# Performance work log

Hardware: AMD Instinct MI355X
Metric: run time of the kernel (lower is better)

## Reference

```python
import jax, jax.numpy as jnp
import numpy as np

B, T, C, H = 8, 1024, 768, 12
HD = C // H  # 64, even for RoPE
ROPE_THETA = 10000.0


def precompute_freqs_cis(dim, end, theta=ROPE_THETA):
    # [end, dim//2, 2] with (cos, sin) in last axis
    freqs = 1.0 / theta ** (jnp.arange(0, dim // 2).astype(jnp.float32) / (dim // 2))
    t = jnp.arange(end)
    f = jnp.outer(t, freqs)
    return jnp.stack([jnp.cos(f), jnp.sin(f)], axis=-1)


def apply_rope(x, fc):
    # x: [B,T,H,hd]; fc: [T,1,hd//2,2] (broadcasts over B and H)
    xr = x.reshape(*x.shape[:-1], -1, 2)
    x_re, x_im = xr[..., 0], xr[..., 1]
    cos, sin = fc[..., 0], fc[..., 1]
    out_re = x_re * cos - x_im * sin
    out_im = x_re * sin + x_im * cos
    return jnp.stack([out_re, out_im], axis=-1).reshape(x.shape)


def setup_inputs() -> dict:
    key = jax.random.key(0)
    k0, k1, k2 = jax.random.split(key, 3)
    x = jax.random.normal(k0, (B, T, C), jnp.float32)
    Wqkv = jax.random.normal(k1, (C, 3 * C), jnp.float32) * 0.02
    bqkv = jnp.zeros((3 * C,), jnp.float32)
    Wproj = jax.random.normal(k2, (C, C), jnp.float32) * 0.02
    bproj = jnp.zeros((C,), jnp.float32)
    mask = jnp.tril(jnp.ones((T, T), jnp.int32))  # causal
    return {"x": x, "Wqkv": Wqkv, "bqkv": bqkv, "Wproj": Wproj, "bproj": bproj, "mask": mask}


def reference(x, Wqkv, bqkv, Wproj, bproj, mask):
    B_, T_, C_ = x.shape
    qkv = (x @ Wqkv + bqkv).reshape(B_, T_, 3, H, HD)
    q, k, v = qkv[:, :, 0], qkv[:, :, 1], qkv[:, :, 2]  # each [B,T,H,hd]
    fc = precompute_freqs_cis(HD, T_)[:, None]  # [T,1,hd//2,2]
    q = apply_rope(q, fc)
    k = apply_rope(k, fc)
    scale = 1.0 / jnp.sqrt(jnp.float32(HD))
    attn = jnp.einsum('bthd,bkhd->bhtk', q, k) * scale  # [B,H,T,T]
    neg = jnp.finfo(attn.dtype).min
    attn = jnp.where(mask[None, None, :, :] == 0, neg, attn)
    attn = jax.nn.softmax(attn, axis=-1)
    out = jnp.einsum('bhtk,bkhd->bthd', attn, v).reshape(B_, T_, C_)
    return out @ Wproj + bproj
```

## Files before the change

kernel.cpp:

```cpp
#include <hip/hip_runtime.h>
#include <cstdint>
#include <cstddef>
#include <cstring>

#define BB 8
#define TT 1024
#define CC 768
#define NH 12
#define HD 64

using bf16x8 = __attribute__((ext_vector_type(8))) short;
using f32x4  = __attribute__((ext_vector_type(4))) float;

static __device__ __forceinline__ short f2bf(float f) {
    uint32_t u;
    __builtin_memcpy(&u, &f, 4);
    u += 0x7FFFu + ((u >> 16) & 1u);
    return (short)(u >> 16);
}

static __device__ __forceinline__ uint32_t bfpack(float lo, float hi) {
    return (uint32_t)(uint16_t)f2bf(lo) | ((uint32_t)(uint16_t)f2bf(hi) << 16);
}

__global__ __launch_bounds__(256)
void prep_kernel(const float* __restrict__ x, const float* __restrict__ Wqkv,
                 const float* __restrict__ Wproj,
                 short* __restrict__ WqkvT, short* __restrict__ WprojT,
                 short* __restrict__ xb, float2* __restrict__ fc) {
    __shared__ float tile[32][33];
    const int tid = threadIdx.x;
    int bid = blockIdx.x;
    if (bid < 2304) {
        const float* in;
        short* out;
        int Cdim, bx, by;
        if (bid < 1728) { in = Wqkv; out = WqkvT; Cdim = 2304; bx = bid % 72; by = bid / 72; }
        else { int b2 = bid - 1728; in = Wproj; out = WprojT; Cdim = 768; bx = b2 % 24; by = b2 / 24; }
        int tx = tid & 31, ty = tid >> 5;
        int c0 = bx * 32, r0 = by * 32;
#pragma unroll
        for (int i = 0; i < 4; i++)
            tile[ty + 8 * i][tx] = in[(size_t)(r0 + ty + 8 * i) * Cdim + c0 + tx];
        __syncthreads();
#pragma unroll
        for (int i = 0; i < 4; i++)
            out[(size_t)(c0 + ty + 8 * i) * 768 + r0 + tx] = f2bf(tile[tx][ty + 8 * i]);
    } else if (bid < 5376) {
        int i = ((bid - 2304) * 256 + tid) * 8;
        float4 f0 = *(const float4*)(x + i);
        float4 f1 = *(const float4*)(x + i + 4);
        bf16x8 h;
        h[0] = f2bf(f0.x); h[1] = f2bf(f0.y); h[2] = f2bf(f0.z); h[3] = f2bf(f0.w);
        h[4] = f2bf(f1.x); h[5] = f2bf(f1.y); h[6] = f2bf(f1.z); h[7] = f2bf(f1.w);
        *(bf16x8*)(xb + i) = h;
    } else {
        int idx = (bid - 5376) * 256 + tid;
        int t = idx >> 5, p = idx & 31;
        float freq = powf(10000.0f, -(float)p / 32.0f);
        float a = (float)t * freq;
        fc[idx] = make_float2(cosf(a), sinf(a));
    }
}

template <int EPI>
__global__ __launch_bounds__(256, 2)
void gemm_kernel(const short* __restrict__ Agl, const short* __restrict__ BT,
                 const float* __restrict__ bias,
                 short* __restrict__ Qb, short* __restrict__ Kb, short* __restrict__ VT,
                 const float2* __restrict__ fc, float* __restrict__ out) {
    __shared__ __align__(16) short smem_s[4 * 128 * 64];
    short (*As)[128 * 64] = (short(*)[128 * 64])smem_s;
    short (*Bs)[128 * 64] = (short(*)[128 * 64])(smem_s + 2 * 128 * 64);
    const int tid = threadIdx.x;
    const int lane = tid & 63, wid = tid >> 6;
    const int g = lane >> 4, c = lane & 15;
    const int wm = wid >> 1, wn = wid & 1;

    const int nx = gridDim.x;
    const int bid = blockIdx.y * nx + blockIdx.x;
    const int cpx = (nx * gridDim.y) >> 3;
    const int swz = (bid & 7) * cpx + (bid >> 3);
    const int m0 = (swz / nx) * 128, n0 = (swz % nx) * 128;

    const int srow = lane >> 2;
    const int sch = lane & 3;
    const short* Ab0 = Agl + (size_t)(m0 + wid * 32 + srow) * 768 + sch * 8;
    const short* Bb0 = BT  + (size_t)(n0 + wid * 32 + srow) * 768 + sch * 8;

    const f32x4 zero4 = {0.f, 0.f, 0.f, 0.f};
    f32x4 acc[4][4];
#pragma unroll
    for (int i = 0; i < 4; i++)
#pragma unroll
        for (int j = 0; j < 4; j++) acc[i][j] = zero4;

    bf16x8 rA[4], rB[4];
#define LOAD(kt)                                                               \
    {                                                                          \
        size_t ko = (size_t)(kt) * 64;                                         \
        _Pragma("unroll")                                                      \
        for (int q = 0; q < 2; q++)                                            \
            _Pragma("unroll")                                                  \
            for (int h = 0; h < 2; h++) {                                      \
                rA[q * 2 + h] = *(const bf16x8*)(Ab0 + (size_t)q * 16 * 768 + ko + h * 32); \
                rB[q * 2 + h] = *(const bf16x8*)(Bb0 + (size_t)q * 16 * 768 + ko + h * 32); \
            }                                                                  \
    }
#define WRITE(buf)                                                             \
    {                                                                          \
        _Pragma("unroll")                                                      \
        for (int q = 0; q < 2; q++)                                            \
            _Pragma("unroll")                                                  \
            for (int h = 0; h < 2; h++) {                                      \
                int row = wid * 32 + q * 16 + srow;                            \
                int ci = sch + h * 4;                                          \
                int idx = row * 64 + ((ci ^ (row & 7)) * 8);                   \
                *(bf16x8*)&As[buf][idx] = rA[q * 2 + h];                       \
                *(bf16x8*)&Bs[buf][idx] = rB[q * 2 + h];                       \
            }                                                                  \
    }
#define COMPUTE(buf)                                                           \
    {                                                                          \
        _Pragma("unroll")                                                      \
        for (int kk = 0; kk < 2; kk++) {                                       \
            bf16x8 af[4], bfr[4];                                              \
            _Pragma("unroll")                                                  \
            for (int mi = 0; mi < 4; mi++) {                                   \
                int row = wm * 64 + mi * 16 + c;                               \
                af[mi] = *(const bf16x8*)&As[buf][row * 64 + (((kk * 4 + g) ^ (row & 7)) * 8)]; \
            }                                                                  \
            _Pragma("unroll")                                                  \
            for (int ni = 0; ni < 4; ni++) {                                   \
                int row = wn * 64 + ni * 16 + c;                               \
                bfr[ni] = *(const bf16x8*)&Bs[buf][row * 64 + (((kk * 4 + g) ^ (row & 7)) * 8)]; \
            }                                                                  \
            __builtin_amdgcn_s_setprio(1);                                     \
            _Pragma("unroll")                                                  \
            for (int mi = 0; mi < 4; mi++)                                     \
                _Pragma("unroll")                                              \
                for (int ni = 0; ni < 4; ni++)                                 \
                    acc[mi][ni] = __builtin_amdgcn_mfma_f32_16x16x32_bf16(     \
                        af[mi], bfr[ni], acc[mi][ni], 0, 0, 0);                \
            __builtin_amdgcn_s_setprio(0);                                     \
        }                                                                      \
    }

    LOAD(0);
    WRITE(0);
    __syncthreads();

#pragma unroll 1
    for (int t2 = 0; t2 < 12; t2 += 2) {
        LOAD(t2 + 1);
        COMPUTE(0);
        __syncthreads();
        WRITE(1);
        __syncthreads();
        if (t2 + 2 < 12) {
            LOAD(t2 + 2);
            COMPUTE(1);
            __syncthreads();
            WRITE(0);
            __syncthreads();
        } else {
            COMPUTE(1);
        }
    }
    __syncthreads();

    if (EPI == 0) {
        uint32_t* LD = (uint32_t*)smem_s;
#pragma unroll
        for (int ni = 0; ni < 4; ni++) {
            int nl = wn * 64 + ni * 16 + c;
            int n = n0 + nl;
            float bv = bias[n];
            int part = (n >= 1536) ? 2 : (n >= 768 ? 1 : 0);
            int d = (n - part * 768) & 63;
#pragma unroll
            for (int mi = 0; mi < 4; mi++) {
#pragma unroll
                for (int r = 0; r < 4; r++) {
                    int ml = wm * 64 + mi * 16 + g * 4 + r;
                    float v = acc[mi][ni][r] + bv;
                    float pv = __shfl_xor(v, 1);
                    if (!(c & 1)) {
                        float o0, o1;
                        if (part < 2) {
                            int t = (m0 + ml) & 1023;
                            float2 cs = fc[t * 32 + (d >> 1)];
                            o0 = v * cs.x - pv * cs.y;
                            o1 = v * cs.y + pv * cs.x;
                            if (part == 0) { o0 *= 0.125f; o1 *= 0.125f; }
                        } else { o0 = v; o1 = pv; }
                        LD[ml * 64 + ((nl >> 1) ^ (((ml >> 2) & 3) << 3))] = bfpack(o0, o1);
                    }
                }
            }
        }
        __syncthreads();
        if (n0 >= 1536) {
            int n0r = n0 - 1536;
            int h0 = n0r >> 6;
            int wc = tid & 63;
            int seg = tid >> 2 >> 4;
            int h = h0 + (wc >> 5);
            int d0 = (2 * wc) & 63;
            int b = m0 >> 10, t0r = m0 & 1023;
            uint32_t wlo[16], whi[16];
#pragma unroll
            for (int j2 = 0; j2 < 16; j2++) {
                int mlA = seg * 32 + 2 * j2;
                int mlB = mlA + 1;
                uint32_t wa = LD[mlA * 64 + (wc ^ (((mlA >> 2) & 3) << 3))];
                uint32_t wb = LD[mlB * 64 + (wc ^ (((mlB >> 2) & 3) << 3))];
                wlo[j2] = (wa & 0xFFFFu) | (wb << 16);
                whi[j2] = (wa >> 16) | (wb & 0xFFFF0000u);
            }
            short* p0 = VT + ((size_t)(b * NH + h) * HD + d0) * TT + t0r + seg * 32;
            short* p1 = p0 + TT;
#pragma unroll
            for (int k = 0; k < 4; k++) {
                int4 v0, v1;
                __builtin_memcpy(&v0, &wlo[k * 4], 16);
                __builtin_memcpy(&v1, &whi[k * 4], 16);
                *(int4*)(p0 + k * 8) = v0;
                *(int4*)(p1 + k * 8) = v1;
            }
        } else {
#pragma unroll
            for (int p = 0; p < 8; p++) {
                int ml = p * 16 + (tid >> 4);
                int wc = (tid & 15) * 4;
                int4 dat = *(const int4*)&LD[ml * 64 + (wc ^ (((ml >> 2) & 3) << 3))];
                int n = n0 + wc * 2;
                int part = (n >= 768) ? 1 : 0;
                int rem = n - part * 768;
                int h = rem >> 6, d = rem & 63;
                int m = m0 + ml, b = m >> 10, t = m & 1023;
                short* dst = (part == 0 ? Qb : Kb)
                             + (((size_t)b * NH + h) * TT + t) * HD + d;
                *(int4*)dst = dat;
            }
        }
    } else {
        float* LDf = (float*)smem_s;
#pragma unroll
        for (int mi = 0; mi < 4; mi++)
#pragma unroll
            for (int ni = 0; ni < 4; ni++) {
                int nl = wn * 64 + ni * 16 + c;
                float bv = bias[n0 + nl];
#pragma unroll
                for (int r = 0; r < 4; r++) {
                    int ml = wm * 64 + mi * 16 + g * 4 + r;
                    LDf[ml * 128 + (nl ^ (r << 3))] = acc[mi][ni][r] + bv;
                }
            }
        __syncthreads();
#pragma unroll
        for (int p = 0; p < 8; p++) {
            int ml = p * 16 + (tid >> 4);
            int rr = (ml & 3) << 3;
            int wc4 = (tid & 15) * 8;
            const float* rp = &LDf[ml * 128 + (wc4 ^ rr)];
            float4 f0 = *(const float4*)rp;
            float4 f1 = *(const float4*)(rp + 4);
            float* dst = out + (size_t)(m0 + ml) * CC + n0 + wc4;
            *(float4*)dst = f0;
            *(float4*)(dst + 4) = f1;
        }
    }
#undef LOAD
#undef WRITE
#undef COMPUTE
}

__global__ __launch_bounds__(256)
void attn_kernel(const short* __restrict__ Qb, const short* __restrict__ Kb,
                 const short* __restrict__ VT, short* __restrict__ Ob) {
    __shared__ uint32_t Pt[4][32][32];
    __shared__ uint32_t ot[128 * 32];
    const int tid = threadIdx.x, lane = tid & 63, wid = tid >> 6;
    const int g = lane >> 4, c = lane & 15;
    const int bh = blockIdx.x, qb = 7 - (int)blockIdx.y;
    const int b = bh / NH, h = bh % NH;
    const short* Qp = Qb + (size_t)bh * TT * HD;
    const short* Kp = Kb + (size_t)bh * TT * HD;
    const short* Vp = VT + (size_t)bh * TT * HD;
    const int q0 = qb * 128 + wid * 32;
    const int sw = (c & 7) << 2;

    bf16x8 qf[2][2];
#pragma unroll
    for (int qs = 0; qs < 2; qs++)
#pragma unroll
        for (int kh = 0; kh < 2; kh++)
            qf[qs][kh] = *(const bf16x8*)(Qp + (size_t)(q0 + qs * 16 + c) * HD + kh * 32 + g * 8);

    const f32x4 zero4 = {0.f, 0.f, 0.f, 0.f};
    f32x4 o[2][4];
#pragma unroll
    for (int qs = 0; qs < 2; qs++)
#pragma unroll
        for (int dt = 0; dt < 4; dt++) o[qs][dt] = zero4;
    float mrun[2] = {-1e30f, -1e30f}, lrun[2] = {0.f, 0.f};

    const int t0max = ((q0 + 31) >> 6) << 6;
    for (int t0 = 0; t0 <= t0max; t0 += 64) {
        f32x4 st[2][4];
#pragma unroll
        for (int nt = 0; nt < 4; nt++) {
            const short* kp = Kp + (size_t)(t0 + nt * 16 + c) * HD + g * 8;
            bf16x8 k0 = *(const bf16x8*)kp;
            bf16x8 k1 = *(const bf16x8*)(kp + 32);
#pragma unroll
            for (int qs = 0; qs < 2; qs++) {
                f32x4 z = zero4;
                __builtin_amdgcn_s_setprio(1);
                z = __builtin_amdgcn_mfma_f32_16x16x32_bf16(k0, qf[qs][0], z, 0, 0, 0);
                z = __builtin_amdgcn_mfma_f32_16x16x32_bf16(k1, qf[qs][1], z, 0, 0, 0);
                __builtin_amdgcn_s_setprio(0);
                st[qs][nt] = z;
            }
        }
        bf16x8 vf[2][4];
#pragma unroll
        for (int blk = 0; blk < 2; blk++)
#pragma unroll
            for (int dt = 0; dt < 4; dt++)
                vf[blk][dt] = *(const bf16x8*)(Vp + (size_t)(dt * 16 + c) * TT + t0 + blk * 32 + g * 8);
        if (t0 + 63 > q0) {
#pragma unroll
            for (int qs = 0; qs < 2; qs++) {
                int q = q0 + qs * 16 + c;
#pragma unroll
                for (int nt = 0; nt < 4; nt++)
#pragma unroll
                    for (int r = 0; r < 4; r++)
                        if (t0 + nt * 16 + g * 4 + r > q) st[qs][nt][r] = -1e30f;
            }
        }
#pragma unroll
        for (int qs = 0; qs < 2; qs++) {
            float mx = st[qs][0][0];
#pragma unroll
            for (int nt = 0; nt < 4; nt++)
#pragma unroll
                for (int r = 0; r < 4; r++) mx = fmaxf(mx, st[qs][nt][r]);
            mx = fmaxf(mx, __shfl_xor(mx, 16));
            mx = fmaxf(mx, __shfl_xor(mx, 32));
            float mnew = fmaxf(mrun[qs], mx);
            float al = __expf(mrun[qs] - mnew);
            mrun[qs] = mnew;
            float sm = 0.f;
#pragma unroll
            for (int nt = 0; nt < 4; nt++)
#pragma unroll
                for (int r = 0; r < 4; r++) {
                    float e = __expf(st[qs][nt][r] - mnew);
                    st[qs][nt][r] = e;
                    sm += e;
                }
            sm += __shfl_xor(sm, 16);
            sm += __shfl_xor(sm, 32);
            lrun[qs] = lrun[qs] * al + sm;
#pragma unroll
            for (int dt = 0; dt < 4; dt++) {
                o[qs][dt][0] *= al; o[qs][dt][1] *= al;
                o[qs][dt][2] *= al; o[qs][dt][3] *= al;
            }
            int row = qs * 16 + c;
#pragma unroll
            for (int nt = 0; nt < 4; nt++) {
                uint32_t w0 = bfpack(st[qs][nt][0], st[qs][nt][1]);
                uint32_t w1 = bfpack(st[qs][nt][2], st[qs][nt][3]);
                int wa = nt * 8 + 2 * g;
                Pt[wid][row][wa ^ sw]       = w0;
                Pt[wid][row][(wa + 1) ^ sw] = w1;
            }
        }
#pragma unroll
        for (int qs = 0; qs < 2; qs++) {
            int row = qs * 16 + c;
#pragma unroll
            for (int blk = 0; blk < 2; blk++) {
                bf16x8 pf = *(const bf16x8*)&Pt[wid][row][(blk * 16 + 4 * g) ^ sw];
                __builtin_amdgcn_s_setprio(1);
#pragma unroll
                for (int dt = 0; dt < 4; dt++)
                    o[qs][dt] = __builtin_amdgcn_mfma_f32_16x16x32_bf16(
                        vf[blk][dt], pf, o[qs][dt], 0, 0, 0);
                __builtin_amdgcn_s_setprio(0);
            }
        }
    }

#pragma unroll
    for (int qs = 0; qs < 2; qs++) {
        float inv = 1.0f / lrun[qs];
        int ql = wid * 32 + qs * 16 + c;
#pragma unroll
        for (int dt = 0; dt < 4; dt++) {
            uint32_t w0 = bfpack(o[qs][dt][0] * inv, o[qs][dt][1] * inv);
            uint32_t w1 = bfpack(o[qs][dt][2] * inv, o[qs][dt][3] * inv);
            int jc0 = dt * 8 + 2 * g;
            int jc1 = jc0 + 1;
            ot[ql * 32 + ((((jc0 >> 2) ^ (c & 7)) << 2) | (jc0 & 3))] = w0;
            ot[ql * 32 + ((((jc1 >> 2) ^ (c & 7)) << 2) | (jc1 & 3))] = w1;
        }
    }
    __syncthreads();
#pragma unroll
    for (int p = 0; p < 4; p++) {
        int q = (tid >> 3) + 32 * p;
        int jb = tid & 7;
        const uint32_t* src = &ot[q * 32 + ((jb ^ (q & 7)) << 2)];
        int4 w = *(const int4*)src;
        *(int4*)(Ob + ((size_t)b * TT + qb * 128 + q) * CC + h * HD + jb * 8) = w;
    }
}

extern "C" void kernel_launch(void* const* d_in, const int* in_sizes, int n_in,
                              void* d_out, int out_size, void* d_ws, size_t ws_size,
                              hipStream_t stream) {
    const float* x     = (const float*)d_in[0];
    const float* Wqkv  = (const float*)d_in[1];
    const float* bqkv  = (const float*)d_in[2];
    const float* Wproj = (const float*)d_in[3];
    const float* bproj = (const float*)d_in[4];

    char* ws = (char*)d_ws;
    short*  WqkvT  = (short*)(ws);
    short*  WprojT = (short*)(ws + 3538944);
    float2* fc     = (float2*)(ws + 3538944 + 1179648);
    short*  Qb     = (short*)(ws + 4980736);
    short*  Kb     = (short*)(ws + 4980736 + 1 * 12582912);
    short*  VOb    = (short*)(ws + 4980736 + 2 * 12582912);
    short*  VbT    = (short*)(ws + 4980736 + 3 * 12582912);
    short*  xb     = VOb;
    float*  out    = (float*)d_out;

    hipLaunchKernelGGL(prep_kernel, dim3(5504), dim3(256), 0, stream,
                       x, Wqkv, Wproj, WqkvT, WprojT, xb, fc);
    hipLaunchKernelGGL((gemm_kernel<0>), dim3(18, 64), dim3(256), 0, stream,
                       xb, WqkvT, bqkv, Qb, Kb, VbT, fc, (float*)nullptr);
    hipLaunchKernelGGL(attn_kernel, dim3(96, 8), dim3(256), 0, stream, Qb, Kb, VbT, VOb);
    hipLaunchKernelGGL((gemm_kernel<1>), dim3(6, 64), dim3(256), 0, stream,
                       VOb, WprojT, bproj,
                       (short*)nullptr, (short*)nullptr, (short*)nullptr,
                       (const float2*)nullptr, out);
}
```

Measured before the change: 164.3 us.

## Load GEMM B-operand fragments directly from global into registers, skip LDS

The GEMM kernel no longer stages the weight (B) tile through shared memory. Each wave loads its own MFMA B fragments straight from global memory into registers, and only A is double-buffered in LDS. That halves the LDS footprint for the QKV GEMM, which now targets 4 blocks per CU instead of 2. In exchange, B data is no longer shared between the two waves that use the same columns, so global/L2 traffic rises, register pressure grows, and the global loads are issued in the same iteration they are consumed, exposing their latency.

Result: slower. 366.1 us (+122.8%).

```diff
diff --git a/kernel.cpp b/kernel.cpp
--- a/kernel.cpp
+++ b/kernel.cpp
@@ -64,14 +64,13 @@
 }
 
 template <int EPI>
-__global__ __launch_bounds__(256, 2)
+__global__ __launch_bounds__(256, EPI == 0 ? 4 : 2)
 void gemm_kernel(const short* __restrict__ Agl, const short* __restrict__ BT,
                  const float* __restrict__ bias,
                  short* __restrict__ Qb, short* __restrict__ Kb, short* __restrict__ VT,
                  const float2* __restrict__ fc, float* __restrict__ out) {
-    __shared__ __align__(16) short smem_s[4 * 128 * 64];
-    short (*As)[128 * 64] = (short(*)[128 * 64])smem_s;
-    short (*Bs)[128 * 64] = (short(*)[128 * 64])(smem_s + 2 * 128 * 64);
+    __shared__ __align__(16) char smem_c[EPI == 0 ? 32768 : 65536];
+    short (*As)[128 * 64] = (short(*)[128 * 64])smem_c;
     const int tid = threadIdx.x;
     const int lane = tid & 63, wid = tid >> 6;
     const int g = lane >> 4, c = lane & 15;
@@ -86,7 +85,7 @@
     const int srow = lane >> 2;
     const int sch = lane & 3;
     const short* Ab0 = Agl + (size_t)(m0 + wid * 32 + srow) * 768 + sch * 8;
-    const short* Bb0 = BT  + (size_t)(n0 + wid * 32 + srow) * 768 + sch * 8;
+    const short* Bw = BT + (size_t)(n0 + wn * 64 + c) * 768 + g * 8;
 
     const f32x4 zero4 = {0.f, 0.f, 0.f, 0.f};
     f32x4 acc[4][4];
@@ -95,19 +94,17 @@
 #pragma unroll
         for (int j = 0; j < 4; j++) acc[i][j] = zero4;
 
-    bf16x8 rA[4], rB[4];
-#define LOAD(kt)                                                               \
+    bf16x8 rA[4], rBf[8];
+#define LOADA(kt)                                                              \
     {                                                                          \
         size_t ko = (size_t)(kt) * 64;                                         \
         _Pragma("unroll")                                                      \
         for (int q = 0; q < 2; q++)                                            \
             _Pragma("unroll")                                                  \
-            for (int h = 0; h < 2; h++) {                                      \
+            for (int h = 0; h < 2; h++)                                        \
                 rA[q * 2 + h] = *(const bf16x8*)(Ab0 + (size_t)q * 16 * 768 + ko + h * 32); \
-                rB[q * 2 + h] = *(const bf16x8*)(Bb0 + (size_t)q * 16 * 768 + ko + h * 32); \
-            }                                                                  \
-    }
-#define WRITE(buf)                                                             \
+    }
+#define WRITEA(buf)                                                            \
     {                                                                          \
         _Pragma("unroll")                                                      \
         for (int q = 0; q < 2; q++)                                            \
@@ -115,25 +112,27 @@
             for (int h = 0; h < 2; h++) {                                      \
                 int row = wid * 32 + q * 16 + srow;                            \
                 int ci = sch + h * 4;                                          \
-                int idx = row * 64 + ((ci ^ (row & 7)) * 8);                   \
-                *(bf16x8*)&As[buf][idx] = rA[q * 2 + h];                       \
-                *(bf16x8*)&Bs[buf][idx] = rB[q * 2 + h];                       \
+                *(bf16x8*)&As[buf][row * 64 + ((ci ^ (row & 7)) * 8)] = rA[q * 2 + h]; \
             }                                                                  \
+    }
+#define LOADB(kt)                                                              \
+    {                                                                          \
+        _Pragma("unroll")                                                      \
+        for (int kk2 = 0; kk2 < 2; kk2++)                                      \
+            _Pragma("unroll")                                                  \
+            for (int ni = 0; ni < 4; ni++)                                     \
+                rBf[kk2 * 4 + ni] = *(const bf16x8*)(Bw + (size_t)ni * 16 * 768 + \
+                                                     (size_t)(kt) * 64 + kk2 * 32); \
     }
 #define COMPUTE(buf)                                                           \
     {                                                                          \
         _Pragma("unroll")                                                      \
         for (int kk = 0; kk < 2; kk++) {                                       \
-            bf16x8 af[4], bfr[4];                                              \
+            bf16x8 af[4];                                                      \
             _Pragma("unroll")                                                  \
             for (int mi = 0; mi < 4; mi++) {                                   \
                 int row = wm * 64 + mi * 16 + c;                               \
                 af[mi] = *(const bf16x8*)&As[buf][row * 64 + (((kk * 4 + g) ^ (row & 7)) * 8)]; \
-            }                                                                  \
-            _Pragma("unroll")                                                  \
-            for (int ni = 0; ni < 4; ni++) {                                   \
-                int row = wn * 64 + ni * 16 + c;                               \
-                bfr[ni] = *(const bf16x8*)&Bs[buf][row * 64 + (((kk * 4 + g) ^ (row & 7)) * 8)]; \
             }                                                                  \
             __builtin_amdgcn_s_setprio(1);                                     \
             _Pragma("unroll")                                                  \
@@ -141,36 +140,39 @@
                 _Pragma("unroll")                                              \
                 for (int ni = 0; ni < 4; ni++)                                 \
                     acc[mi][ni] = __builtin_amdgcn_mfma_f32_16x16x32_bf16(     \
-                        af[mi], bfr[ni], acc[mi][ni], 0, 0, 0);                \
+                        af[mi], rBf[kk * 4 + ni], acc[mi][ni], 0, 0, 0);       \
             __builtin_amdgcn_s_setprio(0);                                     \
         }                                                                      \
     }
 
-    LOAD(0);
-    WRITE(0);
+    LOADA(0);
+    WRITEA(0);
     __syncthreads();
 
 #pragma unroll 1
     for (int t2 = 0; t2 < 12; t2 += 2) {
-        LOAD(t2 + 1);
+        LOADA(t2 + 1);
+        LOADB(t2);
         COMPUTE(0);
         __syncthreads();
-        WRITE(1);
+        WRITEA(1);
         __syncthreads();
         if (t2 + 2 < 12) {
-            LOAD(t2 + 2);
+            LOADA(t2 + 2);
+            LOADB(t2 + 1);
             COMPUTE(1);
             __syncthreads();
-            WRITE(0);
+            WRITEA(0);
             __syncthreads();
         } else {
+            LOADB(t2 + 1);
             COMPUTE(1);
         }
     }
     __syncthreads();
 
     if (EPI == 0) {
-        uint32_t* LD = (uint32_t*)smem_s;
+        uint32_t* LD = (uint32_t*)smem_c;
 #pragma unroll
         for (int ni = 0; ni < 4; ni++) {
             int nl = wn * 64 + ni * 16 + c;
@@ -245,7 +247,7 @@
             }
         }
     } else {
-        float* LDf = (float*)smem_s;
+        float* LDf = (float*)smem_c;
 #pragma unroll
         for (int mi = 0; mi < 4; mi++)
 #pragma unroll
@@ -272,8 +274,9 @@
             *(float4*)(dst + 4) = f1;
         }
     }
-#undef LOAD
-#undef WRITE
+#undef LOADA
+#undef WRITEA
+#undef LOADB
 #undef COMPUTE
 }
 
```
